# Kernel optimization log

Measured on AMD Instinct MI355X. Metric: run time of the kernel, lower is better.

## Reference

```python
import jax, jax.numpy as jnp
import numpy as np

T = 8192   # sequence length (= max_seq_len)
E = 1024   # embedding dim
D = 11     # hard-coded projection dim in source


def setup_inputs() -> dict:
    key = jax.random.key(0)
    ks = jax.random.split(key, 6)
    s_e = 1.0 / np.sqrt(E)
    s_d = 1.0 / np.sqrt(D)
    return {
        "x": jax.random.randint(ks[0], (T,), 0, 32000, dtype=jnp.int64),
        "x_embeddings": jax.random.normal(ks[1], (T, E), dtype=jnp.float32),
        "Wk": jax.random.normal(ks[2], (D, E), dtype=jnp.float32) * s_e,
        "bk": jnp.zeros((D,), dtype=jnp.float32),
        "Wq": jax.random.normal(ks[3], (D, E), dtype=jnp.float32) * s_e,
        "bq": jnp.zeros((D,), dtype=jnp.float32),
        "Wv": jax.random.normal(ks[4], (D, E), dtype=jnp.float32) * s_e,
        "bv": jnp.zeros((D,), dtype=jnp.float32),
        "Wf": jax.random.normal(ks[5], (E, D), dtype=jnp.float32) * s_d,
        "bf": jnp.zeros((E,), dtype=jnp.float32),
    }


def reference(x, x_embeddings, Wk, bk, Wq, bq, Wv, bv, Wf, bf):
    t = x.shape[0]  # static under jit
    k = x_embeddings @ Wk.T + bk            # [T, D]
    q = x_embeddings @ Wq.T + bq            # [T, D]
    v = x_embeddings @ Wv.T + bv            # [T, D]
    att = q @ k.T                           # [T, T]; NOTE: no 1/sqrt(D) scaling in source
    causal = jnp.tril(jnp.ones((t, t), dtype=bool))
    att = jnp.where(causal, att, -jnp.inf)
    att = jax.nn.softmax(att, axis=1)       # dim=1 as in source
    res = att @ v                           # [T, D]
    return res @ Wf.T + bf                  # [T, E]
```

## Files before the change

### kernel.cpp

```cpp
#include <hip/hip_runtime.h>

#define T_SEQ 8192
#define E_DIM 1024
#define QS 36
#define QNEC 8
#define QKC 64
#define QX4 16
#define QXST 17
#define QRB 64
#define AJW 32
#define ABJ 128
#define ARB 256
#define KVW 24
#define TR 16

__device__ __forceinline__ float2 pkfma(float2 a, float2 b, float2 c) {
    return make_float2(fmaf(a.x, b.x, c.x), fmaf(a.y, b.y, c.y));
}
__device__ __forceinline__ float2 f2(float x, float y) { return make_float2(x, y); }

__device__ __forceinline__ void pack3(const float2 o[6], float4* dst) {
    float4 t;
    t.x = o[0].x; t.y = o[0].y; t.z = o[1].x; t.w = o[1].y; dst[0] = t;
    t.x = o[2].x; t.y = o[2].y; t.z = o[3].x; t.w = o[3].y; dst[1] = t;
    t.x = o[4].x; t.y = o[4].y; t.z = o[5].x; t.w = o[5].y; dst[2] = t;
}


__global__ __launch_bounds__(256) void qkv_proj(
    const float* __restrict__ xe,
    const float* __restrict__ Wk, const float* __restrict__ bk,
    const float* __restrict__ Wq, const float* __restrict__ bq,
    const float* __restrict__ Wv, const float* __restrict__ bv,
    float* __restrict__ partQ) {
    const int row0 = blockIdx.x * QRB;
    const int ec = blockIdx.y;
    const int lane = threadIdx.x & 63;
    const int wg = threadIdx.x >> 6;

    __shared__ float4 xT[QRB * QXST];
    __shared__ float4 wT[36 * QX4];

    float2 acc[9];
#pragma unroll
    for (int k = 0; k < 9; ++k) acc[k] = f2(0.f, 0.f);

    for (int cc = 0; cc < 2; ++cc) {
        const int cb = ec * 128 + cc * QKC;
        if (cc) __syncthreads();

#pragma unroll
        for (int t = 0; t < 4; ++t) {
            int idx = threadIdx.x + t * 256;
            int r = idx >> 4, c4 = idx & 15;
            xT[r * QXST + c4] =
                *(const float4*)(xe + (size_t)(row0 + r) * E_DIM + cb + c4 * 4);
        }
        for (int idx = threadIdx.x; idx < 36 * QX4; idx += 256) {
            int r = idx >> 4, c4 = idx & 15;
            float4 v = make_float4(0.f, 0.f, 0.f, 0.f);
            if (r < 33) {
                const float* base = (r < 11) ? (Wk + (size_t)r * E_DIM)
                                  : (r < 22) ? (Wq + (size_t)(r - 11) * E_DIM)
                                             : (Wv + (size_t)(r - 22) * E_DIM);
                v = *(const float4*)(base + cb + c4 * 4);
            }
            wT[idx] = v;
        }
        __syncthreads();

        const float4* xr = xT + lane * QXST;
        const float4* wr = wT + wg * 9 * QX4;
#pragma unroll 4
        for (int c4 = 0; c4 < QX4; ++c4) {
            float4 xv = xr[c4];
#pragma unroll
            for (int k = 0; k < 9; ++k) {
                float4 wv = wr[k * QX4 + c4];
                acc[k] = pkfma(f2(xv.x, xv.y), f2(wv.x, wv.y), acc[k]);
                acc[k] = pkfma(f2(xv.z, xv.w), f2(wv.z, wv.w), acc[k]);
            }
        }
    }

    __syncthreads();
    float* res = (float*)xT;
#pragma unroll
    for (int k = 0; k < 9; ++k) {
        int o = wg * 9 + k;
        bool live = (o < 33);
        int c = (o < 11) ? o : (o < 22) ? o + 1 : (o < 33) ? o + 2
              : (o == 33) ? 11 : (o == 34) ? 23 : 35;
        float b = 0.f;
        if (ec == 0 && live)
            b = (o < 11) ? bk[o] : (o < 22) ? bq[o - 11] : bv[o - 22];
        res[lane * 36 + c] = live ? (acc[k].x + acc[k].y + b) : 0.f;
    }
    __syncthreads();

    float4* dst = (float4*)(partQ + ((size_t)ec * T_SEQ + row0) * QS);
    for (int idx = threadIdx.x; idx < QRB * 9; idx += 256) {
        int r = idx / 9, f = idx % 9;
        dst[idx] = *(const float4*)(res + r * 36 + f * 4);
    }
}

__global__ __launch_bounds__(256) void reduceQ(const float* __restrict__ partQ,
                                               float* __restrict__ qkvF) {
    const size_t idx = (size_t)blockIdx.x * 256 + threadIdx.x;
    const float4* p = (const float4*)partQ;
    const size_t cs = (size_t)T_SEQ * (QS / 4);
    float4 s = make_float4(0.f, 0.f, 0.f, 0.f);
#pragma unroll
    for (int c = 0; c < QNEC; ++c) {
        float4 a = p[idx + (size_t)c * cs];
        s.x += a.x; s.y += a.y; s.z += a.z; s.w += a.w;
    }
    ((float4*)qkvF)[idx] = s;
}

__global__ __launch_bounds__(256) void attn(const float* __restrict__ qkvF,
                                            float* __restrict__ part) {
    const int b = blockIdx.x;
    int rb = 0;
    while ((rb + 1) * (rb + 2) <= b) ++rb;
    const int c = b - rb * (rb + 1);
    const int lane = threadIdx.x & 63;
    const int wid = threadIdx.x >> 6;
    const int r0 = rb * ARB + lane * 4;
    const int j0 = c * ABJ + wid * AJW;

    float2 q[4][6], o[4][6];
#pragma unroll
    for (int i = 0; i < 4; ++i) {
        const float* qp = qkvF + (size_t)(r0 + i) * QS + 12;
#pragma unroll
        for (int d = 0; d < 5; ++d) q[i][d] = f2(qp[2 * d], qp[2 * d + 1]);
        q[i][5] = f2(qp[10], 0.f);
#pragma unroll
        for (int d = 0; d < 6; ++d) o[i][d] = f2(0.f, 0.f);
    }

    __shared__ float kvs[4][AJW * KVW];
    __shared__ float4 red[2][64 * 12];
    float* kv = kvs[wid];

#pragma unroll
    for (int t = 0; t < 3; ++t) {
        int idx = lane + t * 64;
        int row = idx / 6, f = idx % 6;
        int srcOff = f * 4 + (f >= 3 ? 12 : 0);
        float4 v = *(const float4*)(qkvF + (size_t)(j0 + row) * QS + srcOff);
        *(float4*)(kv + row * KVW + f * 4) = v;
    }

    for (int jj = 0; jj < AJW; ++jj) {
        const float* kp = kv + jj * KVW;
        const float4 kA = *(const float4*)(kp);
        const float4 kB = *(const float4*)(kp + 4);
        const float4 kC = *(const float4*)(kp + 8);
        const float4 vA = *(const float4*)(kp + 12);
        const float4 vB = *(const float4*)(kp + 16);
        const float4 vC = *(const float4*)(kp + 20);
        const float2 k01 = f2(kA.x, kA.y), k23 = f2(kA.z, kA.w);
        const float2 k45 = f2(kB.x, kB.y), k67 = f2(kB.z, kB.w);
        const float2 k89 = f2(kC.x, kC.y), kXp = f2(kC.z, kC.w);
        const int j = j0 + jj;

#pragma unroll
        for (int i = 0; i < 4; ++i) {
            float2 s = pkfma(q[i][0], k01, pkfma(q[i][1], k23, pkfma(q[i][2], k45,
                       pkfma(q[i][3], k67, pkfma(q[i][4], k89,
                       pkfma(q[i][5], kXp, f2(0.f, 0.f)))))));
            float pe = __expf(s.x + s.y);
            pe = (j <= r0 + i) ? pe : 0.f;
            float2 p2 = f2(pe, pe);
            o[i][0] = pkfma(p2, f2(vA.x, vA.y), o[i][0]);
            o[i][1] = pkfma(p2, f2(vA.z, vA.w), o[i][1]);
            o[i][2] = pkfma(p2, f2(vB.x, vB.y), o[i][2]);
            o[i][3] = pkfma(p2, f2(vB.z, vB.w), o[i][3]);
            o[i][4] = pkfma(p2, f2(vC.x, vC.y), o[i][4]);
            o[i][5] = pkfma(p2, f2(vC.z, 1.f),  o[i][5]);
        }
    }

    __syncthreads();
    if (wid >= 2) {
        float4* dst = red[wid - 2] + lane * 12;
#pragma unroll
        for (int i = 0; i < 4; ++i) pack3(o[i], dst + i * 3);
    }
    __syncthreads();
    if (wid < 2) {
        const float4* src = red[wid] + lane * 12;
#pragma unroll
        for (int i = 0; i < 4; ++i) {
            float4 s0 = src[i * 3 + 0], s1 = src[i * 3 + 1], s2 = src[i * 3 + 2];
            o[i][0].x += s0.x; o[i][0].y += s0.y; o[i][1].x += s0.z; o[i][1].y += s0.w;
            o[i][2].x += s1.x; o[i][2].y += s1.y; o[i][3].x += s1.z; o[i][3].y += s1.w;
            o[i][4].x += s2.x; o[i][4].y += s2.y; o[i][5].x += s2.z; o[i][5].y += s2.w;
        }
    }
    __syncthreads();
    if (wid == 1) {
        float4* dst = red[0] + lane * 12;
#pragma unroll
        for (int i = 0; i < 4; ++i) pack3(o[i], dst + i * 3);
    }
    __syncthreads();
    if (wid == 0) {
        const float4* src = red[0] + lane * 12;
#pragma unroll
        for (int i = 0; i < 4; ++i) {
            float4 s0 = src[i * 3 + 0], s1 = src[i * 3 + 1], s2 = src[i * 3 + 2];
            o[i][0].x += s0.x; o[i][0].y += s0.y; o[i][1].x += s0.z; o[i][1].y += s0.w;
            o[i][2].x += s1.x; o[i][2].y += s1.y; o[i][3].x += s1.z; o[i][3].y += s1.w;
            o[i][4].x += s2.x; o[i][4].y += s2.y; o[i][5].x += s2.z; o[i][5].y += s2.w;
        }
        float* d0 = part + ((size_t)c * T_SEQ + r0) * 12;
#pragma unroll
        for (int i = 0; i < 4; ++i) pack3(o[i], (float4*)(d0 + i * 12));
    }
}

__global__ __launch_bounds__(256) void pass2(const float* __restrict__ part,
                                             const float* __restrict__ Wf,
                                             const float* __restrict__ bf,
                                             float* __restrict__ out) {
    const int t0 = blockIdx.x * TR;
    const int cnt = 2 * (t0 / ARB) + 2;
    __shared__ float red[16][16][12];
    __shared__ float res[TR][12];
    {
        const int r = threadIdx.x >> 4;
        const int s = threadIdx.x & 15;
        float a[12];
#pragma unroll
        for (int d = 0; d < 12; ++d) a[d] = 0.f;
        const size_t S = (size_t)T_SEQ * 12;
        const float* p = part + (size_t)(t0 + r) * 12;
        for (int c = s; c < cnt; c += 16) {
            const float4* pc = (const float4*)(p + (size_t)c * S);
            float4 x0 = pc[0], x1 = pc[1], x2 = pc[2];
            a[0] += x0.x; a[1] += x0.y; a[2]  += x0.z; a[3]  += x0.w;
            a[4] += x1.x; a[5] += x1.y; a[6]  += x1.z; a[7]  += x1.w;
            a[8] += x2.x; a[9] += x2.y; a[10] += x2.z; a[11] += x2.w;
        }
#pragma unroll
        for (int d = 0; d < 12; ++d) red[r][s][d] = a[d];
    }
    __syncthreads();
    if (threadIdx.x < TR * 12) {
        const int r = threadIdx.x / 12, d = threadIdx.x % 12;
        float sum = 0.f;
#pragma unroll
        for (int s = 0; s < 16; ++s) sum += red[r][s][d];
        res[r][d] = (d == 11) ? (1.f / sum) : sum;
    }
    __syncthreads();

    const int e0 = threadIdx.x * 4;
    float w[4][11];
    const float* wp = Wf + (size_t)e0 * 11;
#pragma unroll
    for (int ee = 0; ee < 4; ++ee)
#pragma unroll
        for (int i = 0; i < 11; ++i) w[ee][i] = wp[ee * 11 + i];
    const float4 bv = *(const float4*)(bf + e0);

    for (int r = 0; r < TR; ++r) {
        float rr[12];
#pragma unroll
        for (int d = 0; d < 12; ++d) rr[d] = res[r][d];
        float2 a0 = f2(0.f, 0.f), a1 = a0, a2 = a0, a3 = a0;
#pragma unroll
        for (int d = 0; d < 10; d += 2) {
            float2 rv = f2(rr[d], rr[d + 1]);
            a0 = pkfma(rv, f2(w[0][d], w[0][d + 1]), a0);
            a1 = pkfma(rv, f2(w[1][d], w[1][d + 1]), a1);
            a2 = pkfma(rv, f2(w[2][d], w[2][d + 1]), a2);
            a3 = pkfma(rv, f2(w[3][d], w[3][d + 1]), a3);
        }
        const float rl = rr[11];
        float4 ov;
        ov.x = (a0.x + a0.y + rr[10] * w[0][10]) * rl + bv.x;
        ov.y = (a1.x + a1.y + rr[10] * w[1][10]) * rl + bv.y;
        ov.z = (a2.x + a2.y + rr[10] * w[2][10]) * rl + bv.z;
        ov.w = (a3.x + a3.y + rr[10] * w[3][10]) * rl + bv.w;
        *(float4*)(out + (size_t)(t0 + r) * E_DIM + e0) = ov;
    }
}

extern "C" void kernel_launch(void* const* d_in, const int* in_sizes, int n_in,
                              void* d_out, int out_size, void* d_ws, size_t ws_size,
                              hipStream_t stream) {
    const float* xe = (const float*)d_in[1];
    const float* Wk = (const float*)d_in[2];
    const float* bk = (const float*)d_in[3];
    const float* Wq = (const float*)d_in[4];
    const float* bq = (const float*)d_in[5];
    const float* Wv = (const float*)d_in[6];
    const float* bv = (const float*)d_in[7];
    const float* Wf = (const float*)d_in[8];
    const float* bf = (const float*)d_in[9];
    float* out = (float*)d_out;

    float* qkvF  = (float*)d_ws;
    float* partQ = qkvF + (size_t)T_SEQ * QS;
    float* part  = partQ;

    qkv_proj<<<dim3(T_SEQ / QRB, QNEC), 256, 0, stream>>>(xe, Wk, bk, Wq, bq, Wv, bv, partQ);
    reduceQ<<<(T_SEQ * QS / 4) / 256, 256, 0, stream>>>(partQ, qkvF);
    const int nrg = T_SEQ / ARB;
    attn<<<nrg * (nrg + 1), 256, 0, stream>>>(qkvF, part);
    pass2<<<T_SEQ / TR, 256, 0, stream>>>(part, Wf, bf, out);
}
```

Measured before the change: 169.0 us.

## Retile QKV projection over more row/K-chunks and double attention waves per block

The QKV projection now handles 128 rows per block with two accumulator sets per thread over 32-wide K chunks, and it splits E into 16 partial slices instead of 8. The attention kernel goes to 512 threads, with 8 waves each covering 16 keys, and gains an extra level in the shared-memory tree reduction. The aim is more parallelism per block and better reuse of weights in registers. The cost is twice the partial-sum traffic into reduceQ, more reduction barriers in attention, and higher register pressure.

```diff
diff --git a/kernel.cpp b/kernel.cpp
--- a/kernel.cpp
+++ b/kernel.cpp
@@ -3,12 +3,12 @@
 #define T_SEQ 8192
 #define E_DIM 1024
 #define QS 36
-#define QNEC 8
-#define QKC 64
-#define QX4 16
-#define QXST 17
-#define QRB 64
-#define AJW 32
+#define QNEC 16
+#define QKC 32
+#define QX4 8
+#define QXST 9
+#define QRB 128
+#define AJW 16
 #define ABJ 128
 #define ARB 256
 #define KVW 24
@@ -41,23 +41,25 @@
     __shared__ float4 xT[QRB * QXST];
     __shared__ float4 wT[36 * QX4];
 
-    float2 acc[9];
-#pragma unroll
-    for (int k = 0; k < 9; ++k) acc[k] = f2(0.f, 0.f);
+    float2 acc[2][9];
+#pragma unroll
+    for (int u = 0; u < 2; ++u)
+#pragma unroll
+        for (int k = 0; k < 9; ++k) acc[u][k] = f2(0.f, 0.f);
 
     for (int cc = 0; cc < 2; ++cc) {
-        const int cb = ec * 128 + cc * QKC;
+        const int cb = ec * 64 + cc * QKC;
         if (cc) __syncthreads();
 
 #pragma unroll
         for (int t = 0; t < 4; ++t) {
             int idx = threadIdx.x + t * 256;
-            int r = idx >> 4, c4 = idx & 15;
+            int r = idx >> 3, c4 = idx & 7;
             xT[r * QXST + c4] =
                 *(const float4*)(xe + (size_t)(row0 + r) * E_DIM + cb + c4 * 4);
         }
         for (int idx = threadIdx.x; idx < 36 * QX4; idx += 256) {
-            int r = idx >> 4, c4 = idx & 15;
+            int r = idx >> 3, c4 = idx & 7;
             float4 v = make_float4(0.f, 0.f, 0.f, 0.f);
             if (r < 33) {
                 const float* base = (r < 11) ? (Wk + (size_t)r * E_DIM)
@@ -71,14 +73,18 @@
 
         const float4* xr = xT + lane * QXST;
         const float4* wr = wT + wg * 9 * QX4;
-#pragma unroll 4
+#pragma unroll
         for (int c4 = 0; c4 < QX4; ++c4) {
-            float4 xv = xr[c4];
+            float4 xv0 = xr[c4];
+            float4 xv1 = xr[64 * QXST + c4];
 #pragma unroll
             for (int k = 0; k < 9; ++k) {
                 float4 wv = wr[k * QX4 + c4];
-                acc[k] = pkfma(f2(xv.x, xv.y), f2(wv.x, wv.y), acc[k]);
-                acc[k] = pkfma(f2(xv.z, xv.w), f2(wv.z, wv.w), acc[k]);
+                float2 wlo = f2(wv.x, wv.y), whi = f2(wv.z, wv.w);
+                acc[0][k] = pkfma(f2(xv0.x, xv0.y), wlo, acc[0][k]);
+                acc[0][k] = pkfma(f2(xv0.z, xv0.w), whi, acc[0][k]);
+                acc[1][k] = pkfma(f2(xv1.x, xv1.y), wlo, acc[1][k]);
+                acc[1][k] = pkfma(f2(xv1.z, xv1.w), whi, acc[1][k]);
             }
         }
     }
@@ -94,7 +100,8 @@
         float b = 0.f;
         if (ec == 0 && live)
             b = (o < 11) ? bk[o] : (o < 22) ? bq[o - 11] : bv[o - 22];
-        res[lane * 36 + c] = live ? (acc[k].x + acc[k].y + b) : 0.f;
+        res[lane * 36 + c]        = live ? (acc[0][k].x + acc[0][k].y + b) : 0.f;
+        res[(lane + 64) * 36 + c] = live ? (acc[1][k].x + acc[1][k].y + b) : 0.f;
     }
     __syncthreads();
 
@@ -119,7 +126,7 @@
     ((float4*)qkvF)[idx] = s;
 }
 
-__global__ __launch_bounds__(256) void attn(const float* __restrict__ qkvF,
+__global__ __launch_bounds__(512) void attn(const float* __restrict__ qkvF,
                                             float* __restrict__ part) {
     const int b = blockIdx.x;
     int rb = 0;
@@ -130,6 +137,9 @@
     const int r0 = rb * ARB + lane * 4;
     const int j0 = c * ABJ + wid * AJW;
 
+    __shared__ float sh[12288];
+    float* kv = sh + wid * (AJW * KVW);
+
     float2 q[4][6], o[4][6];
 #pragma unroll
     for (int i = 0; i < 4; ++i) {
@@ -141,17 +151,15 @@
         for (int d = 0; d < 6; ++d) o[i][d] = f2(0.f, 0.f);
     }
 
-    __shared__ float kvs[4][AJW * KVW];
-    __shared__ float4 red[2][64 * 12];
-    float* kv = kvs[wid];
-
-#pragma unroll
-    for (int t = 0; t < 3; ++t) {
+#pragma unroll
+    for (int t = 0; t < 2; ++t) {
         int idx = lane + t * 64;
-        int row = idx / 6, f = idx % 6;
-        int srcOff = f * 4 + (f >= 3 ? 12 : 0);
-        float4 v = *(const float4*)(qkvF + (size_t)(j0 + row) * QS + srcOff);
-        *(float4*)(kv + row * KVW + f * 4) = v;
+        if (idx < AJW * 6) {
+            int row = idx / 6, f = idx % 6;
+            int srcOff = f * 4 + (f >= 3 ? 12 : 0);
+            float4 v = *(const float4*)(qkvF + (size_t)(j0 + row) * QS + srcOff);
+            *(float4*)(kv + row * KVW + f * 4) = v;
+        }
     }
 
     for (int jj = 0; jj < AJW; ++jj) {
@@ -184,15 +192,16 @@
         }
     }
 
-    __syncthreads();
-    if (wid >= 2) {
-        float4* dst = red[wid - 2] + lane * 12;
+    float4* red = (float4*)sh;
+    __syncthreads();
+    if (wid >= 4) {
+        float4* dst = red + (size_t)(wid - 4) * 768 + lane * 12;
 #pragma unroll
         for (int i = 0; i < 4; ++i) pack3(o[i], dst + i * 3);
     }
     __syncthreads();
-    if (wid < 2) {
-        const float4* src = red[wid] + lane * 12;
+    if (wid < 4) {
+        const float4* src = red + (size_t)wid * 768 + lane * 12;
 #pragma unroll
         for (int i = 0; i < 4; ++i) {
             float4 s0 = src[i * 3 + 0], s1 = src[i * 3 + 1], s2 = src[i * 3 + 2];
@@ -202,14 +211,31 @@
         }
     }
     __syncthreads();
+    if (wid == 2 || wid == 3) {
+        float4* dst = red + (size_t)(wid - 2) * 768 + lane * 12;
+#pragma unroll
+        for (int i = 0; i < 4; ++i) pack3(o[i], dst + i * 3);
+    }
+    __syncthreads();
+    if (wid < 2) {
+        const float4* src = red + (size_t)wid * 768 + lane * 12;
+#pragma unroll
+        for (int i = 0; i < 4; ++i) {
+            float4 s0 = src[i * 3 + 0], s1 = src[i * 3 + 1], s2 = src[i * 3 + 2];
+            o[i][0].x += s0.x; o[i][0].y += s0.y; o[i][1].x += s0.z; o[i][1].y += s0.w;
+            o[i][2].x += s1.x; o[i][2].y += s1.y; o[i][3].x += s1.z; o[i][3].y += s1.w;
+            o[i][4].x += s2.x; o[i][4].y += s2.y; o[i][5].x += s2.z; o[i][5].y += s2.w;
+        }
+    }
+    __syncthreads();
     if (wid == 1) {
-        float4* dst = red[0] + lane * 12;
+        float4* dst = red + lane * 12;
 #pragma unroll
         for (int i = 0; i < 4; ++i) pack3(o[i], dst + i * 3);
     }
     __syncthreads();
     if (wid == 0) {
-        const float4* src = red[0] + lane * 12;
+        const float4* src = red + lane * 12;
 #pragma unroll
         for (int i = 0; i < 4; ++i) {
             float4 s0 = src[i * 3 + 0], s1 = src[i * 3 + 1], s2 = src[i * 3 + 2];
@@ -312,6 +338,6 @@
     qkv_proj<<<dim3(T_SEQ / QRB, QNEC), 256, 0, stream>>>(xe, Wk, bk, Wq, bq, Wv, bv, partQ);
     reduceQ<<<(T_SEQ * QS / 4) / 256, 256, 0, stream>>>(partQ, qkvF);
     const int nrg = T_SEQ / ARB;
-    attn<<<nrg * (nrg + 1), 256, 0, stream>>>(qkvF, part);
+    attn<<<nrg * (nrg + 1), 512, 0, stream>>>(qkvF, part);
     pass2<<<T_SEQ / TR, 256, 0, stream>>>(part, Wf, bf, out);
 }
```

Result: slower. 176.2 us (+4.2%).

## Halve attention key chunk size to double block count and restructure reduction

Applied to the files above, without the earlier changes.

Attention blocks now cover 64 keys instead of 128 (16 per wave), doubling the grid to 2112 blocks and the number of partial outputs that pass2 must sum. The cross-wave reduction is rewritten as a pairwise chain through one shared buffer laid out with a 64-float4 stride per component, which should avoid bank conflicts and cut shared memory use. The aim is more parallelism and occupancy in the attention phase. The cost is twice the partial-result traffic and a longer reduction in pass2, plus shorter inner loops with more fixed overhead per block.

```diff
diff --git a/kernel.cpp b/kernel.cpp
--- a/kernel.cpp
+++ b/kernel.cpp
@@ -8,8 +8,8 @@
 #define QX4 16
 #define QXST 17
 #define QRB 64
-#define AJW 32
-#define ABJ 128
+#define AJW 16
+#define ABJ 64
 #define ARB 256
 #define KVW 24
 #define TR 16
@@ -19,11 +19,23 @@
 }
 __device__ __forceinline__ float2 f2(float x, float y) { return make_float2(x, y); }
 
+__device__ __forceinline__ void pack3s(const float2 o[6], float4* dst) {
+    float4 t;
+    t.x = o[0].x; t.y = o[0].y; t.z = o[1].x; t.w = o[1].y; dst[0]   = t;
+    t.x = o[2].x; t.y = o[2].y; t.z = o[3].x; t.w = o[3].y; dst[64]  = t;
+    t.x = o[4].x; t.y = o[4].y; t.z = o[5].x; t.w = o[5].y; dst[128] = t;
+}
 __device__ __forceinline__ void pack3(const float2 o[6], float4* dst) {
     float4 t;
     t.x = o[0].x; t.y = o[0].y; t.z = o[1].x; t.w = o[1].y; dst[0] = t;
     t.x = o[2].x; t.y = o[2].y; t.z = o[3].x; t.w = o[3].y; dst[1] = t;
     t.x = o[4].x; t.y = o[4].y; t.z = o[5].x; t.w = o[5].y; dst[2] = t;
+}
+__device__ __forceinline__ void add3s(float2 o[6], const float4* src) {
+    float4 s0 = src[0], s1 = src[64], s2 = src[128];
+    o[0].x += s0.x; o[0].y += s0.y; o[1].x += s0.z; o[1].y += s0.w;
+    o[2].x += s1.x; o[2].y += s1.y; o[3].x += s1.z; o[3].y += s1.w;
+    o[4].x += s2.x; o[4].y += s2.y; o[5].x += s2.z; o[5].y += s2.w;
 }
 
 
@@ -123,13 +135,16 @@
                                             float* __restrict__ part) {
     const int b = blockIdx.x;
     int rb = 0;
-    while ((rb + 1) * (rb + 2) <= b) ++rb;
-    const int c = b - rb * (rb + 1);
+    while (2 * (rb + 1) * (rb + 2) <= b) ++rb;
+    const int c = b - 2 * rb * (rb + 1);
     const int lane = threadIdx.x & 63;
     const int wid = threadIdx.x >> 6;
     const int r0 = rb * ARB + lane * 4;
     const int j0 = c * ABJ + wid * AJW;
 
+    __shared__ float sh[3072];
+    float* kv = sh + wid * (AJW * KVW);
+
     float2 q[4][6], o[4][6];
 #pragma unroll
     for (int i = 0; i < 4; ++i) {
@@ -141,17 +156,15 @@
         for (int d = 0; d < 6; ++d) o[i][d] = f2(0.f, 0.f);
     }
 
-    __shared__ float kvs[4][AJW * KVW];
-    __shared__ float4 red[2][64 * 12];
-    float* kv = kvs[wid];
-
-#pragma unroll
-    for (int t = 0; t < 3; ++t) {
+#pragma unroll
+    for (int t = 0; t < 2; ++t) {
         int idx = lane + t * 64;
-        int row = idx / 6, f = idx % 6;
-        int srcOff = f * 4 + (f >= 3 ? 12 : 0);
-        float4 v = *(const float4*)(qkvF + (size_t)(j0 + row) * QS + srcOff);
-        *(float4*)(kv + row * KVW + f * 4) = v;
+        if (idx < AJW * 6) {
+            int row = idx / 6, f = idx % 6;
+            int srcOff = f * 4 + (f >= 3 ? 12 : 0);
+            float4 v = *(const float4*)(qkvF + (size_t)(j0 + row) * QS + srcOff);
+            *(float4*)(kv + row * KVW + f * 4) = v;
+        }
     }
 
     for (int jj = 0; jj < AJW; ++jj) {
@@ -184,39 +197,36 @@
         }
     }
 
-    __syncthreads();
-    if (wid >= 2) {
-        float4* dst = red[wid - 2] + lane * 12;
-#pragma unroll
-        for (int i = 0; i < 4; ++i) pack3(o[i], dst + i * 3);
-    }
-    __syncthreads();
-    if (wid < 2) {
-        const float4* src = red[wid] + lane * 12;
-#pragma unroll
-        for (int i = 0; i < 4; ++i) {
-            float4 s0 = src[i * 3 + 0], s1 = src[i * 3 + 1], s2 = src[i * 3 + 2];
-            o[i][0].x += s0.x; o[i][0].y += s0.y; o[i][1].x += s0.z; o[i][1].y += s0.w;
-            o[i][2].x += s1.x; o[i][2].y += s1.y; o[i][3].x += s1.z; o[i][3].y += s1.w;
-            o[i][4].x += s2.x; o[i][4].y += s2.y; o[i][5].x += s2.z; o[i][5].y += s2.w;
-        }
-    }
+    float4* buf = (float4*)sh;
     __syncthreads();
     if (wid == 1) {
-        float4* dst = red[0] + lane * 12;
-#pragma unroll
-        for (int i = 0; i < 4; ++i) pack3(o[i], dst + i * 3);
+#pragma unroll
+        for (int i = 0; i < 4; ++i) pack3s(o[i], buf + (i * 3) * 64 + lane);
     }
     __syncthreads();
     if (wid == 0) {
-        const float4* src = red[0] + lane * 12;
-#pragma unroll
-        for (int i = 0; i < 4; ++i) {
-            float4 s0 = src[i * 3 + 0], s1 = src[i * 3 + 1], s2 = src[i * 3 + 2];
-            o[i][0].x += s0.x; o[i][0].y += s0.y; o[i][1].x += s0.z; o[i][1].y += s0.w;
-            o[i][2].x += s1.x; o[i][2].y += s1.y; o[i][3].x += s1.z; o[i][3].y += s1.w;
-            o[i][4].x += s2.x; o[i][4].y += s2.y; o[i][5].x += s2.z; o[i][5].y += s2.w;
-        }
+#pragma unroll
+        for (int i = 0; i < 4; ++i) add3s(o[i], buf + (i * 3) * 64 + lane);
+    }
+    __syncthreads();
+    if (wid == 3) {
+#pragma unroll
+        for (int i = 0; i < 4; ++i) pack3s(o[i], buf + (i * 3) * 64 + lane);
+    }
+    __syncthreads();
+    if (wid == 2) {
+#pragma unroll
+        for (int i = 0; i < 4; ++i) add3s(o[i], buf + (i * 3) * 64 + lane);
+    }
+    __syncthreads();
+    if (wid == 2) {
+#pragma unroll
+        for (int i = 0; i < 4; ++i) pack3s(o[i], buf + (i * 3) * 64 + lane);
+    }
+    __syncthreads();
+    if (wid == 0) {
+#pragma unroll
+        for (int i = 0; i < 4; ++i) add3s(o[i], buf + (i * 3) * 64 + lane);
         float* d0 = part + ((size_t)c * T_SEQ + r0) * 12;
 #pragma unroll
         for (int i = 0; i < 4; ++i) pack3(o[i], (float4*)(d0 + i * 12));
@@ -228,7 +238,7 @@
                                              const float* __restrict__ bf,
                                              float* __restrict__ out) {
     const int t0 = blockIdx.x * TR;
-    const int cnt = 2 * (t0 / ARB) + 2;
+    const int cnt = 4 * (t0 / ARB) + 4;
     __shared__ float red[16][16][12];
     __shared__ float res[TR][12];
     {
@@ -311,7 +321,6 @@
 
     qkv_proj<<<dim3(T_SEQ / QRB, QNEC), 256, 0, stream>>>(xe, Wk, bk, Wq, bq, Wv, bv, partQ);
     reduceQ<<<(T_SEQ * QS / 4) / 256, 256, 0, stream>>>(partQ, qkvF);
-    const int nrg = T_SEQ / ARB;
-    attn<<<nrg * (nrg + 1), 256, 0, stream>>>(qkvF, part);
+    attn<<<2112, 256, 0, stream>>>(qkvF, part);
     pass2<<<T_SEQ / TR, 256, 0, stream>>>(part, Wf, bf, out);
 }
```

Measured after the change: 163.8 us. 1.03x faster.
